# Performance work log

Hardware: AMD Instinct MI355X
Metric: run time of the kernel (lower is better)

Reference implementation:

```python
import jax, jax.numpy as jnp
import numpy as np

B, S, D, K = 32, 1024, 256, 1024
DECAY = 0.99
EPS = 1e-05          # EMA laplace epsilon
LN_EPS = 1e-05       # LayerNorm epsilon
COMMITMENT_COST = 0.25


def setup_inputs() -> dict:
    key = jax.random.key(0)
    k1, k2, k3 = jax.random.split(key, 3)
    inputs = jax.random.normal(k1, (B, S, D), jnp.float32)
    # nn.Embedding init: uniform(-1/K, 1/K)
    weight = jax.random.uniform(k2, (K, D), jnp.float32, -1.0 / K, 1.0 / K)
    ema_w = jax.random.normal(k3, (K, D), jnp.float32)
    ema_cluster_size = jnp.zeros((K,), jnp.float32)
    ln_gamma = jnp.ones((D,), jnp.float32)
    ln_beta = jnp.zeros((D,), jnp.float32)
    return {"inputs": inputs, "weight": weight, "ema_w": ema_w,
            "ema_cluster_size": ema_cluster_size,
            "ln_gamma": ln_gamma, "ln_beta": ln_beta}


def _layernorm(x, g, b):
    mu = jnp.mean(x, axis=-1, keepdims=True)
    var = jnp.mean((x - mu) ** 2, axis=-1, keepdims=True)
    return (x - mu) * jax.lax.rsqrt(var + LN_EPS) * g + b


def reference(inputs, weight, ema_w, ema_cluster_size, ln_gamma, ln_beta):
    flat_input = inputs.reshape(-1, D)          # [N, D] (unnormalized, used for EMA dw)
    feats = _layernorm(flat_input, ln_gamma, ln_beta)  # norm_input in sample()

    # euclidean distances ||f||^2 + ||w||^2 - 2 f w^T  -> [N, K]
    d = (jnp.sum(feats ** 2, axis=1, keepdims=True)
         + jnp.sum(weight ** 2, axis=1)
         - 2.0 * feats @ weight.T)

    sampled_dist = jnp.min(d, axis=1)           # [N]
    idx_flat = jnp.argmin(d, axis=1)            # [N] int

    # faithful reproduction of the source's reordering:
    # argsort per batch row (values in [0,S)) then flat-index into the [N]-long index vector
    order = jnp.argsort(sampled_dist.reshape(B, S), axis=1).reshape(-1)  # [N], values in [0,S)
    enc_idx = idx_flat[order]                   # [N]

    quantized = weight[enc_idx].reshape(B, S, D)

    # ---- EMA codebook update (training path), no gradients ----
    fi = jax.lax.stop_gradient(flat_input)
    counts = jax.ops.segment_sum(jnp.ones((B * S,), jnp.float32), enc_idx,
                                 num_segments=K)                    # encodings.sum(0)
    new_cs = ema_cluster_size * DECAY + (1.0 - DECAY) * counts
    n = jnp.sum(new_cs)
    new_cs = (new_cs + EPS) / (n + K * EPS) * n
    dw = jax.ops.segment_sum(fi, enc_idx, num_segments=K)            # encodings.T @ flat_input
    new_ema_w = jax.lax.stop_gradient(ema_w) * DECAY + (1.0 - DECAY) * dw
    new_weight = new_ema_w / new_cs[:, None]

    # ---- losses (avg=False, loss_type=0) ----
    e_latent = jnp.mean((jax.lax.stop_gradient(quantized) - inputs) ** 2)
    q_latent = jnp.mean((quantized - jax.lax.stop_gradient(inputs)) ** 2)
    loss = q_latent + COMMITMENT_COST * e_latent

    # straight-through estimator
    quantized_st = inputs + jax.lax.stop_gradient(quantized - inputs)

    avg_probs = counts / (B * S)
    perplexity = jnp.exp(-jnp.sum(avg_probs * jnp.log(avg_probs + 1e-10)))

    return quantized_st, loss, perplexity, enc_idx, new_weight, new_ema_w, new_cs
```

## Files before the change

kernel.cpp:

```cpp
#include <hip/hip_runtime.h>
#include <cmath>

#define B_ 32
#define S_ 1024
#define D_ 256
#define K_ 1024
#define N_ (B_*S_)

#define O_Q     0
#define O_LOSS  8388608
#define O_PERP  8388609
#define O_IDX   8388610
#define O_NW    8421378
#define O_NEW   8683522
#define O_NCS   8945666

#define OFF_FH    0ull
#define OFF_WH    16777216ull
#define OFF_BW    17301504ull
#define OFF_BWF   17309696ull
#define OFF_SAMP  17313792ull
#define OFF_IDXF  17575936ull
#define OFF_ENC   17707008ull
#define OFF_CNT   17838080ull
#define OFF_SLOWC 17842176ull
#define OFF_SLOWL 17842240ull
#define OFF_LOSSP 17973312ull
#define OFF_COFF  18235456ull
#define OFF_CUR   18239552ull
#define OFF_ROWL  18243648ull
#define OFF_MUIV  18374720ull
#define OFF_AR    18636864ull
#define OFF_NTOT  18899008ull

#define MARGIN 4e-5f

typedef _Float16 f16x8 __attribute__((ext_vector_type(8)));
typedef _Float16 f16x4 __attribute__((ext_vector_type(4)));
typedef float    f32x4 __attribute__((ext_vector_type(4)));

#define GL16(gp, lp) __builtin_amdgcn_global_load_lds( \
    (const __attribute__((address_space(1))) unsigned int*)(const void*)(gp), \
    (__attribute__((address_space(3))) unsigned int*)(void*)(lp), 16, 0, 0)

__global__ void k_pre(const float* __restrict__ x, const float* __restrict__ gam,
                      const float* __restrict__ bet, _Float16* __restrict__ fh,
                      const float* __restrict__ w, double* __restrict__ Bw,
                      float* __restrict__ Bwf, _Float16* __restrict__ wh,
                      float2* __restrict__ muiv, double* __restrict__ Ar,
                      unsigned* __restrict__ cnt, unsigned* __restrict__ slowC) {
    int lane = threadIdx.x & 63, wv = threadIdx.x >> 6;
    if (blockIdx.x < N_ / 4) {
        int n = blockIdx.x * 4 + wv;
        const float4 xv = ((const float4*)(x + (size_t)n * D_))[lane];
        const float4 gv = ((const float4*)gam)[lane];
        const float4 bv = ((const float4*)bet)[lane];
        float s = xv.x + xv.y + xv.z + xv.w;
        for (int m = 32; m > 0; m >>= 1) s += __shfl_xor(s, m, 64);
        float mu = s * (1.0f / 256.0f);
        float c0 = xv.x - mu, c1 = xv.y - mu, c2 = xv.z - mu, c3 = xv.w - mu;
        float vs = c0 * c0 + c1 * c1 + c2 * c2 + c3 * c3;
        for (int m = 32; m > 0; m >>= 1) vs += __shfl_xor(vs, m, 64);
        float inv = 1.0f / sqrtf(vs * (1.0f / 256.0f) + 1e-5f);
        float f0 = c0 * inv * gv.x + bv.x;
        float f1 = c1 * inv * gv.y + bv.y;
        float f2 = c2 * inv * gv.z + bv.z;
        float f3 = c3 * inv * gv.w + bv.w;
        double a = (double)f0 * f0 + (double)f1 * f1
                 + (double)f2 * f2 + (double)f3 * f3;
        for (int m = 32; m > 0; m >>= 1) a += __shfl_xor(a, m, 64);
        f16x4 o;
        o[0] = (_Float16)f0; o[1] = (_Float16)f1;
        o[2] = (_Float16)f2; o[3] = (_Float16)f3;
        *(f16x4*)&fh[(size_t)n * D_ + lane * 4] = o;
        if (lane == 0) { muiv[n] = make_float2(mu, inv); Ar[n] = a; }
    } else if (blockIdx.x < N_ / 4 + K_ / 4) {
        int k = (blockIdx.x - N_ / 4) * 4 + wv;
        const float4 v = ((const float4*)(w + (size_t)k * D_))[lane];
        double s = (double)v.x * v.x + (double)v.y * v.y
                 + (double)v.z * v.z + (double)v.w * v.w;
        for (int m = 32; m > 0; m >>= 1) s += __shfl_xor(s, m, 64);
        f16x4 o;
        o[0] = (_Float16)v.x; o[1] = (_Float16)v.y;
        o[2] = (_Float16)v.z; o[3] = (_Float16)v.w;
        *(f16x4*)&wh[(size_t)k * D_ + lane * 4] = o;
        if (lane == 0) { Bw[k] = s; Bwf[k] = (float)s; }
    } else {
        int t = threadIdx.x;
#pragma unroll
        for (int i = 0; i < 4; i++) cnt[t + i * 256] = 0u;
        if (t == 0) *slowC = 0u;
    }
}

__launch_bounds__(512, 4)
__global__ void k_phase1(const _Float16* __restrict__ fh, const _Float16* __restrict__ wh,
                         const float* __restrict__ Bwf, float* __restrict__ pq) {
    __shared__ __align__(16) _Float16 sA[3][128][32];
    __shared__ __align__(16) _Float16 sB[3][256][32];

    const int tid = threadIdx.x;
    const int lane = tid & 63;
    const int w = tid >> 6;
    const int wr = w >> 2;
    const int wc = w & 3;
    const int l15 = lane & 15;
    const int g = lane >> 4;
    const int id = blockIdx.x;
    const int grp = (id & 7) * 32 + (id >> 5);
    const int chunk = (id >> 3) & 3;
    const int row0 = grp * 128;
    const int c0 = chunk * 256;

    const int srow = lane >> 2;
    const int scol = (lane & 3) * 8;
    const _Float16* gp[3];
    int lrow[3]; int isA[3];
#pragma unroll
    for (int j = 0; j < 3; j++) {
        int li = w * 3 + j;
        if (li < 8) {
            isA[j] = 1; lrow[j] = li * 16;
            gp[j] = fh + (size_t)(row0 + li * 16 + srow) * 256 + scol;
        } else {
            isA[j] = 0; lrow[j] = (li - 8) * 16;
            gp[j] = wh + (size_t)(c0 + (li - 8) * 16 + srow) * 256 + scol;
        }
    }

    f32x4 acc[4][4];
#pragma unroll
    for (int a = 0; a < 4; a++)
#pragma unroll
        for (int b = 0; b < 4; b++) acc[a][b] = (f32x4){0.f, 0.f, 0.f, 0.f};

#define STAGE(bi, kk) do { \
    const int eoff_ = (kk) * 32; \
    _Pragma("unroll") \
    for (int j_ = 0; j_ < 3; j_++) { \
        if (isA[j_]) GL16(gp[j_] + eoff_, &sA[bi][lrow[j_]][0]); \
        else         GL16(gp[j_] + eoff_, &sB[bi][lrow[j_]][0]); \
    } \
} while (0)

    STAGE(0, 0);
    STAGE(1, 1);
    asm volatile("s_waitcnt vmcnt(3)" ::: "memory");
    __builtin_amdgcn_s_barrier();
    __builtin_amdgcn_sched_barrier(0);

#pragma unroll
    for (int ks = 0; ks < 8; ks++) {
        const int cur = ks % 3;
        if (ks < 6) STAGE((ks + 2) % 3, ks + 2);

        f16x8 cfr[4];
#pragma unroll
        for (int cb = 0; cb < 4; cb++)
            cfr[cb] = *(const f16x8*)&sB[cur][wc * 64 + cb * 16 + l15][g * 8];
        __builtin_amdgcn_s_setprio(1);
#pragma unroll
        for (int rb = 0; rb < 4; rb++) {
            f16x8 rf = *(const f16x8*)&sA[cur][wr * 64 + rb * 16 + l15][g * 8];
#pragma unroll
            for (int cb = 0; cb < 4; cb++)
                acc[cb][rb] = __builtin_amdgcn_mfma_f32_16x16x32_f16(
                    cfr[cb], rf, acc[cb][rb], 0, 0, 0);
        }
        __builtin_amdgcn_s_setprio(0);
        __builtin_amdgcn_sched_barrier(0);

        if (ks < 6)       asm volatile("s_waitcnt vmcnt(3)" ::: "memory");
        else if (ks == 6) asm volatile("s_waitcnt vmcnt(0)" ::: "memory");
        if (ks < 7) {
            __builtin_amdgcn_s_barrier();
            __builtin_amdgcn_sched_barrier(0);
        }
    }
#undef STAGE
    __syncthreads();

    float bwv[4][4];
#pragma unroll
    for (int cb = 0; cb < 4; cb++)
#pragma unroll
        for (int r = 0; r < 4; r++)
            bwv[cb][r] = Bwf[c0 + wc * 64 + cb * 16 + g * 4 + r];

    float* red = (float*)&sA[0][0][0];
#pragma unroll
    for (int rb = 0; rb < 4; rb++) {
        float m1 = 3e38f, m2 = 3e38f; int c1 = 0x7fffffff;
#pragma unroll
        for (int cb = 0; cb < 4; cb++) {
#pragma unroll
            for (int r = 0; r < 4; r++) {
                float sv = fmaf(-2.0f, acc[cb][rb][r], bwv[cb][r]);
                int c = c0 + wc * 64 + cb * 16 + g * 4 + r;
                if (sv < m1 || (sv == m1 && c < c1)) { m2 = m1; m1 = sv; c1 = c; }
                else if (sv < m2) m2 = sv;
            }
        }
#pragma unroll
        for (int msk = 16; msk <= 32; msk <<= 1) {
            float om1 = __shfl_xor(m1, msk, 64);
            float om2 = __shfl_xor(m2, msk, 64);
            int   oc  = __shfl_xor(c1, msk, 64);
            if (om1 < m1 || (om1 == m1 && oc < c1)) {
                m2 = (m1 < om2) ? m1 : om2; m1 = om1; c1 = oc;
            } else {
                m2 = (om1 < m2) ? om1 : m2;
            }
        }
        if (lane < 16) {
            int rl = wr * 64 + rb * 16 + l15;
            int base = (rl * 4 + wc) * 3;
            red[base] = m1; red[base + 1] = m2; ((int*)red)[base + 2] = c1;
        }
    }
    __syncthreads();
    if (tid < 128) {
        float M1 = 3e38f, M2 = 3e38f; int C1 = 0x7fffffff;
        for (int q = 0; q < 4; q++) {
            int base = (tid * 4 + q) * 3;
            float m1 = red[base], m2 = red[base + 1]; int c = ((int*)red)[base + 2];
            if (m1 < M1 || (m1 == M1 && c < C1)) {
                M2 = (M1 < m2) ? M1 : m2; M1 = m1; C1 = c;
            } else {
                M2 = (m1 < M2) ? m1 : M2;
            }
        }
        pq[chunk * N_ + row0 + tid] = M1;
        pq[4 * N_ + chunk * N_ + row0 + tid] = M2;
        ((int*)pq)[8 * N_ + chunk * N_ + row0 + tid] = C1;
    }
}

__global__ void k_phase2(const float* __restrict__ x, const float* __restrict__ gam,
                         const float* __restrict__ bet, const float* __restrict__ w,
                         const double* __restrict__ Bw, const float* __restrict__ pq,
                         const float2* __restrict__ muiv, const double* __restrict__ Ar,
                         double* __restrict__ sampled, int* __restrict__ idxf,
                         unsigned* __restrict__ slowC, int* __restrict__ slowL) {
    int lane = threadIdx.x & 63, wv = threadIdx.x >> 6;
    int n = blockIdx.x * 4 + wv;
    const float* pm1 = pq;
    const float* pm2 = pq + 4 * N_;
    const int*   pc1 = (const int*)pq + 8 * N_;
    float M1 = 3e38f, M2 = 3e38f; int C1 = 0x7fffffff;
#pragma unroll
    for (int c = 0; c < 4; c++) {
        float m1 = pm1[c * N_ + n], m2 = pm2[c * N_ + n]; int cc = pc1[c * N_ + n];
        if (m1 < M1 || (m1 == M1 && cc < C1)) {
            M2 = (M1 < m2) ? M1 : m2; M1 = m1; C1 = cc;
        } else {
            M2 = (m1 < M2) ? m1 : M2;
        }
    }
    if (M2 - M1 <= MARGIN) {
        if (lane == 0) { unsigned p = atomicAdd(slowC, 1u); slowL[p] = n; }
        return;
    }
    float2 mi = muiv[n];
    double mu = mi.x, inv = mi.y;
    double A = Ar[n];
    const float* row = x + (size_t)n * D_;
    const float* wr_ = w + (size_t)C1 * D_;
    double ss = 0.0;
#pragma unroll
    for (int i = 0; i < 4; i++) {
        int d = lane + 64 * i;
        double f = ((double)row[d] - mu) * inv * (double)gam[d] + (double)bet[d];
        ss += f * (double)wr_[d];
    }
    for (int m = 32; m > 0; m >>= 1) ss += __shfl_xor(ss, m, 64);
    if (lane == 0) { sampled[n] = (A + Bw[C1]) - 2.0 * ss; idxf[n] = C1; }
}

__launch_bounds__(256)
__global__ void k_slow(const float* __restrict__ x, const float* __restrict__ gam,
                       const float* __restrict__ bet, const float* __restrict__ w,
                       const double* __restrict__ Bw,
                       const float2* __restrict__ muiv, const double* __restrict__ Ar,
                       const int* __restrict__ slowL, const unsigned* __restrict__ slowC,
                       double* __restrict__ sampled, int* __restrict__ idxf) {
    __shared__ double sf[256];
    __shared__ double bmW[4];
    __shared__ int    bcW[4];
    int tid = threadIdx.x, lane = tid & 63, wv = tid >> 6;
    int cnt = (int)*slowC;
    for (int it = blockIdx.x; it < cnt; it += gridDim.x) {
        int n = slowL[it];
        float2 mi = muiv[n];
        double mu = mi.x, inv = mi.y;
        double A = Ar[n];
        double f = ((double)x[(size_t)n * D_ + tid] - mu) * inv
                   * (double)gam[tid] + (double)bet[tid];
        sf[tid] = f;
        __syncthreads();

        double bm = 1.0e300; int bc = 0x7fffffff;
        for (int r = 0; r < 4; r++) {
            int cc = r * 256 + wv * 64 + lane;
            const float* wr = w + (size_t)cc * D_;
            double acc = 0.0;
#pragma unroll 8
            for (int d4 = 0; d4 < 64; d4++) {
                float4 w4 = *(const float4*)(wr + d4 * 4);
                acc += sf[d4 * 4] * (double)w4.x + sf[d4 * 4 + 1] * (double)w4.y
                     + sf[d4 * 4 + 2] * (double)w4.z + sf[d4 * 4 + 3] * (double)w4.w;
            }
            double dist = (A + Bw[cc]) - 2.0 * acc;
            if (dist < bm) { bm = dist; bc = cc; }
        }
        for (int m = 32; m > 0; m >>= 1) {
            double om = __shfl_xor(bm, m, 64);
            int    oc = __shfl_xor(bc, m, 64);
            if (om < bm || (om == bm && oc < bc)) { bm = om; bc = oc; }
        }
        if (lane == 0) { bmW[wv] = bm; bcW[wv] = bc; }
        __syncthreads();
        if (tid == 0) {
            double M = bmW[0]; int C = bcW[0];
            for (int i = 1; i < 4; i++)
                if (bmW[i] < M || (bmW[i] == M && bcW[i] < C)) { M = bmW[i]; C = bcW[i]; }
            sampled[n] = M; idxf[n] = C;
        }
        __syncthreads();
    }
}

__launch_bounds__(256)
__global__ void k_rank(const double* __restrict__ sampled, const int* __restrict__ idxf,
                       int* __restrict__ enc) {
    __shared__ double val[1024];
    int b = blockIdx.x >> 2;
    int q = blockIdx.x & 3;
    int t = threadIdx.x;
    size_t base = (size_t)b * S_;
#pragma unroll
    for (int e = 0; e < 4; e++)
        val[t + e * 256] = sampled[base + t + e * 256];
    __syncthreads();
    int i = q * 256 + t;
    double vi = val[i];
    int rank = 0;
#pragma unroll 8
    for (int j = 0; j < 1024; j++) {
        double vj = val[j];
        rank += (vj < vi) || (vj == vi && j < i);
    }
    enc[base + rank] = idxf[i];
}

__global__ void k_gather(const float* __restrict__ x, const float* __restrict__ w,
                         const int* __restrict__ enc, float* __restrict__ out,
                         unsigned* __restrict__ cnt, double* __restrict__ lossP) {
    int lane = threadIdx.x & 63, wv = threadIdx.x >> 6;
    int n = blockIdx.x * 4 + wv;
    int e = enc[n];
    const float4 q4 = ((const float4*)(w + (size_t)e * D_))[lane];
    const float4 x4 = ((const float4*)(x + (size_t)n * D_))[lane];
    ((float4*)(out + O_Q + (size_t)n * D_))[lane] = q4;
    double d0 = (double)q4.x - (double)x4.x;
    double d1 = (double)q4.y - (double)x4.y;
    double d2 = (double)q4.z - (double)x4.z;
    double d3 = (double)q4.w - (double)x4.w;
    double ls = d0 * d0 + d1 * d1 + d2 * d2 + d3 * d3;
    for (int m = 32; m > 0; m >>= 1) ls += __shfl_xor(ls, m, 64);
    if (lane == 0) {
        lossP[n] = ls;
        out[O_IDX + n] = (float)e;
        atomicAdd(&cnt[e], 1u);
    }
}

__launch_bounds__(1024)
__global__ void k_scan(const unsigned* __restrict__ cnt, const float* __restrict__ ema_cs,
                       int* __restrict__ coff, int* __restrict__ cur,
                       double* __restrict__ ntotP) {
    __shared__ int tmp[1024];
    __shared__ double redn[16];
    int t = threadIdx.x;
    int my = (int)cnt[t];
    tmp[t] = my;
    double part = (double)(0.99f * ema_cs[t] + 0.01f * (float)my);
    __syncthreads();
    for (int off = 1; off < 1024; off <<= 1) {
        int v = (t >= off) ? tmp[t - off] : 0;
        __syncthreads();
        tmp[t] += v;
        __syncthreads();
    }
    int excl = tmp[t] - my;
    coff[t] = excl;
    cur[t] = excl;
    for (int m = 32; m > 0; m >>= 1) part += __shfl_xor(part, m, 64);
    if ((t & 63) == 0) redn[t >> 6] = part;
    __syncthreads();
    if (t == 0) {
        double s = 0.0;
        for (int i = 0; i < 16; i++) s += redn[i];
        *ntotP = s;
    }
}

__global__ void k_scatter(const int* __restrict__ enc, int* __restrict__ cur,
                          int* __restrict__ rowl) {
    int n = blockIdx.x * 256 + threadIdx.x;
    int e = enc[n];
    int p = atomicAdd(&cur[e], 1);
    rowl[p] = n;
}

__launch_bounds__(256)
__global__ void k_post(const unsigned* __restrict__ cnt, const float* __restrict__ ema_cs,
                       const double* __restrict__ lossP,
                       const int* __restrict__ coff, const int* __restrict__ rowl,
                       const float* __restrict__ x, const float* __restrict__ ema_w,
                       const double* __restrict__ ntotP, float* __restrict__ out) {
    __shared__ double redd[24];
    int tid = threadIdx.x;
    double ntot = *ntotP;

    if (blockIdx.x < K_) {
        int k = blockIdx.x;
        float cs0 = 0.99f * ema_cs[k] + 0.01f * (float)cnt[k];
        double csf = ((double)cs0 + 1e-5) / (ntot + 1024.0 * 1e-5) * ntot;
        int base = coff[k];
        int c = (int)cnt[k];
        float acc = 0.0f;
        int j = 0;
        for (; j + 8 <= c; j += 8) {
            int r[8];
#pragma unroll
            for (int u = 0; u < 8; u++) r[u] = rowl[base + j + u];
            float v[8];
#pragma unroll
            for (int u = 0; u < 8; u++) v[u] = x[(size_t)r[u] * D_ + tid];
#pragma unroll
            for (int u = 0; u < 8; u++) acc += v[u];
        }
        for (; j < c; j++) acc += x[(size_t)rowl[base + j] * D_ + tid];
        size_t idx = (size_t)k * D_ + tid;
        float ne = 0.99f * ema_w[idx] + 0.01f * acc;
        out[O_NEW + idx] = ne;
        out[O_NW + idx] = ne / (float)csf;
    } else {
        for (int i = tid; i < K_; i += 256) {
            float cs0 = 0.99f * ema_cs[i] + 0.01f * (float)cnt[i];
            double c2 = ((double)cs0 + 1e-5) / (ntot + 1024.0 * 1e-5) * ntot;
            out[O_NCS + i] = (float)c2;
        }
        double ent = 0.0;
        for (int i = tid; i < K_; i += 256) {
            double p = (double)cnt[i] / 32768.0;
            ent += -p * log(p + 1e-10);
        }
        for (int m = 32; m > 0; m >>= 1) ent += __shfl_xor(ent, m, 64);
        if ((tid & 63) == 0) redd[8 + (tid >> 6)] = ent;
        double ls = 0.0;
        for (int i = tid; i < N_; i += 256) ls += lossP[i];
        for (int m = 32; m > 0; m >>= 1) ls += __shfl_xor(ls, m, 64);
        if ((tid & 63) == 0) redd[16 + (tid >> 6)] = ls;
        __syncthreads();
        if (tid == 0) {
            double e = redd[8] + redd[9] + redd[10] + redd[11];
            double l = redd[16] + redd[17] + redd[18] + redd[19];
            out[O_PERP] = (float)exp(e);
            out[O_LOSS] = (float)(1.25 * l / 8388608.0);
        }
    }
}

extern "C" void kernel_launch(void* const* d_in, const int* in_sizes, int n_in,
                              void* d_out, int out_size, void* d_ws, size_t ws_size,
                              hipStream_t stream) {
    (void)in_sizes; (void)n_in; (void)out_size; (void)ws_size;
    const float* x      = (const float*)d_in[0];
    const float* w      = (const float*)d_in[1];
    const float* ema_w  = (const float*)d_in[2];
    const float* ema_cs = (const float*)d_in[3];
    const float* g      = (const float*)d_in[4];
    const float* bt     = (const float*)d_in[5];
    float* out = (float*)d_out;
    char* ws = (char*)d_ws;

    _Float16* fh = (_Float16*)(ws + OFF_FH);
    _Float16* wh = (_Float16*)(ws + OFF_WH);
    double* Bw   = (double*)(ws + OFF_BW);
    float*  Bwf  = (float*)(ws + OFF_BWF);
    double* samp = (double*)(ws + OFF_SAMP);
    int*    idxf = (int*)(ws + OFF_IDXF);
    int*    enc  = (int*)(ws + OFF_ENC);
    unsigned* cnt = (unsigned*)(ws + OFF_CNT);
    unsigned* slowC = (unsigned*)(ws + OFF_SLOWC);
    int*    slowL = (int*)(ws + OFF_SLOWL);
    double* lossP = (double*)(ws + OFF_LOSSP);
    int*    coff  = (int*)(ws + OFF_COFF);
    int*    cur   = (int*)(ws + OFF_CUR);
    int*    rowl  = (int*)(ws + OFF_ROWL);
    float2* muiv  = (float2*)(ws + OFF_MUIV);
    double* Ar    = (double*)(ws + OFF_AR);
    double* ntotP = (double*)(ws + OFF_NTOT);

    k_pre<<<N_ / 4 + K_ / 4 + 1, 256, 0, stream>>>(x, g, bt, fh, w, Bw, Bwf, wh,
                                                   muiv, Ar, cnt, slowC);
    k_phase1<<<1024, 512, 0, stream>>>(fh, wh, Bwf, out);
    k_phase2<<<N_ / 4, 256, 0, stream>>>(x, g, bt, w, Bw, out, muiv, Ar,
                                         samp, idxf, slowC, slowL);
    k_slow<<<2048, 256, 0, stream>>>(x, g, bt, w, Bw, muiv, Ar, slowL, slowC, samp, idxf);
    k_rank<<<B_ * 4, 256, 0, stream>>>(samp, idxf, enc);
    k_gather<<<N_ / 4, 256, 0, stream>>>(x, w, enc, out, cnt, lossP);
    k_scan<<<1, 1024, 0, stream>>>(cnt, ema_cs, coff, cur, ntotP);
    k_scatter<<<N_ / 256, 256, 0, stream>>>(enc, cur, rowl);
    k_post<<<K_ + 1, 256, 0, stream>>>(cnt, ema_cs, lossP, coff, rowl, x, ema_w,
                                       ntotP, out);
}
```

Measured before the change: 279.5 us.

## Fold slow-path rescoring into phase2 and merge scatter into scan kernel

The separate k_slow kernel, its atomic worklist and counter are removed. Ambiguous rows (top-2 gap within the margin) are now rescored exactly in fp64 by the same wavefront in k_phase2, with each lane scanning 16 codewords. The k_scatter kernel is folded into the single-block scan kernel, which now uses LDS atomics for the bucket cursors. This cuts two kernel launches and the global atomics, but a wave that hits the slow path stalls its block, and the scatter of 32K rows now runs serially in one workgroup.

```diff
diff --git a/kernel.cpp b/kernel.cpp
--- a/kernel.cpp
+++ b/kernel.cpp
@@ -23,11 +23,8 @@
 #define OFF_IDXF  17575936ull
 #define OFF_ENC   17707008ull
 #define OFF_CNT   17838080ull
-#define OFF_SLOWC 17842176ull
-#define OFF_SLOWL 17842240ull
 #define OFF_LOSSP 17973312ull
 #define OFF_COFF  18235456ull
-#define OFF_CUR   18239552ull
 #define OFF_ROWL  18243648ull
 #define OFF_MUIV  18374720ull
 #define OFF_AR    18636864ull
@@ -48,7 +45,7 @@
                       const float* __restrict__ w, double* __restrict__ Bw,
                       float* __restrict__ Bwf, _Float16* __restrict__ wh,
                       float2* __restrict__ muiv, double* __restrict__ Ar,
-                      unsigned* __restrict__ cnt, unsigned* __restrict__ slowC) {
+                      unsigned* __restrict__ cnt) {
     int lane = threadIdx.x & 63, wv = threadIdx.x >> 6;
     if (blockIdx.x < N_ / 4) {
         int n = blockIdx.x * 4 + wv;
@@ -89,7 +86,6 @@
         int t = threadIdx.x;
 #pragma unroll
         for (int i = 0; i < 4; i++) cnt[t + i * 256] = 0u;
-        if (t == 0) *slowC = 0u;
     }
 }
 
@@ -236,12 +232,13 @@
     }
 }
 
+__launch_bounds__(256)
 __global__ void k_phase2(const float* __restrict__ x, const float* __restrict__ gam,
                          const float* __restrict__ bet, const float* __restrict__ w,
                          const double* __restrict__ Bw, const float* __restrict__ pq,
                          const float2* __restrict__ muiv, const double* __restrict__ Ar,
-                         double* __restrict__ sampled, int* __restrict__ idxf,
-                         unsigned* __restrict__ slowC, int* __restrict__ slowL) {
+                         double* __restrict__ sampled, int* __restrict__ idxf) {
+    __shared__ double sf[4][256];
     int lane = threadIdx.x & 63, wv = threadIdx.x >> 6;
     int n = blockIdx.x * 4 + wv;
     const float* pm1 = pq;
@@ -257,60 +254,40 @@
             M2 = (m1 < M2) ? m1 : M2;
         }
     }
-    if (M2 - M1 <= MARGIN) {
-        if (lane == 0) { unsigned p = atomicAdd(slowC, 1u); slowL[p] = n; }
-        return;
-    }
     float2 mi = muiv[n];
     double mu = mi.x, inv = mi.y;
     double A = Ar[n];
     const float* row = x + (size_t)n * D_;
-    const float* wr_ = w + (size_t)C1 * D_;
-    double ss = 0.0;
-#pragma unroll
-    for (int i = 0; i < 4; i++) {
-        int d = lane + 64 * i;
-        double f = ((double)row[d] - mu) * inv * (double)gam[d] + (double)bet[d];
-        ss += f * (double)wr_[d];
-    }
-    for (int m = 32; m > 0; m >>= 1) ss += __shfl_xor(ss, m, 64);
-    if (lane == 0) { sampled[n] = (A + Bw[C1]) - 2.0 * ss; idxf[n] = C1; }
-}
-
-__launch_bounds__(256)
-__global__ void k_slow(const float* __restrict__ x, const float* __restrict__ gam,
-                       const float* __restrict__ bet, const float* __restrict__ w,
-                       const double* __restrict__ Bw,
-                       const float2* __restrict__ muiv, const double* __restrict__ Ar,
-                       const int* __restrict__ slowL, const unsigned* __restrict__ slowC,
-                       double* __restrict__ sampled, int* __restrict__ idxf) {
-    __shared__ double sf[256];
-    __shared__ double bmW[4];
-    __shared__ int    bcW[4];
-    int tid = threadIdx.x, lane = tid & 63, wv = tid >> 6;
-    int cnt = (int)*slowC;
-    for (int it = blockIdx.x; it < cnt; it += gridDim.x) {
-        int n = slowL[it];
-        float2 mi = muiv[n];
-        double mu = mi.x, inv = mi.y;
-        double A = Ar[n];
-        double f = ((double)x[(size_t)n * D_ + tid] - mu) * inv
-                   * (double)gam[tid] + (double)bet[tid];
-        sf[tid] = f;
-        __syncthreads();
-
+
+    if (M2 - M1 > MARGIN) {
+        const float* wr_ = w + (size_t)C1 * D_;
+        double ss = 0.0;
+#pragma unroll
+        for (int i = 0; i < 4; i++) {
+            int d = lane + 64 * i;
+            double f = ((double)row[d] - mu) * inv * (double)gam[d] + (double)bet[d];
+            ss += f * (double)wr_[d];
+        }
+        for (int m = 32; m > 0; m >>= 1) ss += __shfl_xor(ss, m, 64);
+        if (lane == 0) { sampled[n] = (A + Bw[C1]) - 2.0 * ss; idxf[n] = C1; }
+    } else {
+#pragma unroll
+        for (int i = 0; i < 4; i++) {
+            int d = lane + 64 * i;
+            sf[wv][d] = ((double)row[d] - mu) * inv * (double)gam[d] + (double)bet[d];
+        }
         double bm = 1.0e300; int bc = 0x7fffffff;
-        for (int r = 0; r < 4; r++) {
-            int cc = r * 256 + wv * 64 + lane;
+        for (int k = 0; k < 16; k++) {
+            int cc = lane * 16 + k;
             const float* wr = w + (size_t)cc * D_;
-            double acc = 0.0;
+            double acc2 = 0.0;
 #pragma unroll 8
             for (int d4 = 0; d4 < 64; d4++) {
                 float4 w4 = *(const float4*)(wr + d4 * 4);
-                acc += sf[d4 * 4] * (double)w4.x + sf[d4 * 4 + 1] * (double)w4.y
-                     + sf[d4 * 4 + 2] * (double)w4.z + sf[d4 * 4 + 3] * (double)w4.w;
+                acc2 += sf[wv][d4 * 4] * (double)w4.x + sf[wv][d4 * 4 + 1] * (double)w4.y
+                      + sf[wv][d4 * 4 + 2] * (double)w4.z + sf[wv][d4 * 4 + 3] * (double)w4.w;
             }
-            double dist = (A + Bw[cc]) - 2.0 * acc;
+            double dist = (A + Bw[cc]) - 2.0 * acc2;
             if (dist < bm) { bm = dist; bc = cc; }
         }
         for (int m = 32; m > 0; m >>= 1) {
@@ -318,15 +295,7 @@
             int    oc = __shfl_xor(bc, m, 64);
             if (om < bm || (om == bm && oc < bc)) { bm = om; bc = oc; }
         }
-        if (lane == 0) { bmW[wv] = bm; bcW[wv] = bc; }
-        __syncthreads();
-        if (tid == 0) {
-            double M = bmW[0]; int C = bcW[0];
-            for (int i = 1; i < 4; i++)
-                if (bmW[i] < M || (bmW[i] == M && bcW[i] < C)) { M = bmW[i]; C = bcW[i]; }
-            sampled[n] = M; idxf[n] = C;
-        }
-        __syncthreads();
+        if (lane == 0) { sampled[n] = bm; idxf[n] = bc; }
     }
 }
 
@@ -376,10 +345,11 @@
 }
 
 __launch_bounds__(1024)
-__global__ void k_scan(const unsigned* __restrict__ cnt, const float* __restrict__ ema_cs,
-                       int* __restrict__ coff, int* __restrict__ cur,
-                       double* __restrict__ ntotP) {
+__global__ void k_scansc(const unsigned* __restrict__ cnt, const float* __restrict__ ema_cs,
+                         const int* __restrict__ enc, int* __restrict__ coff,
+                         int* __restrict__ rowl, double* __restrict__ ntotP) {
     __shared__ int tmp[1024];
+    __shared__ int curL[1024];
     __shared__ double redn[16];
     int t = threadIdx.x;
     int my = (int)cnt[t];
@@ -394,7 +364,7 @@
     }
     int excl = tmp[t] - my;
     coff[t] = excl;
-    cur[t] = excl;
+    curL[t] = excl;
     for (int m = 32; m > 0; m >>= 1) part += __shfl_xor(part, m, 64);
     if ((t & 63) == 0) redn[t >> 6] = part;
     __syncthreads();
@@ -403,14 +373,12 @@
         for (int i = 0; i < 16; i++) s += redn[i];
         *ntotP = s;
     }
-}
-
-__global__ void k_scatter(const int* __restrict__ enc, int* __restrict__ cur,
-                          int* __restrict__ rowl) {
-    int n = blockIdx.x * 256 + threadIdx.x;
-    int e = enc[n];
-    int p = atomicAdd(&cur[e], 1);
-    rowl[p] = n;
+    for (int it = 0; it < 32; it++) {
+        int i = it * 1024 + t;
+        int e = enc[i];
+        int p = atomicAdd(&curL[e], 1);
+        rowl[p] = i;
+    }
 }
 
 __launch_bounds__(256)
@@ -494,26 +462,20 @@
     int*    idxf = (int*)(ws + OFF_IDXF);
     int*    enc  = (int*)(ws + OFF_ENC);
     unsigned* cnt = (unsigned*)(ws + OFF_CNT);
-    unsigned* slowC = (unsigned*)(ws + OFF_SLOWC);
-    int*    slowL = (int*)(ws + OFF_SLOWL);
     double* lossP = (double*)(ws + OFF_LOSSP);
     int*    coff  = (int*)(ws + OFF_COFF);
-    int*    cur   = (int*)(ws + OFF_CUR);
     int*    rowl  = (int*)(ws + OFF_ROWL);
     float2* muiv  = (float2*)(ws + OFF_MUIV);
     double* Ar    = (double*)(ws + OFF_AR);
     double* ntotP = (double*)(ws + OFF_NTOT);
 
     k_pre<<<N_ / 4 + K_ / 4 + 1, 256, 0, stream>>>(x, g, bt, fh, w, Bw, Bwf, wh,
-                                                   muiv, Ar, cnt, slowC);
+                                                   muiv, Ar, cnt);
     k_phase1<<<1024, 512, 0, stream>>>(fh, wh, Bwf, out);
-    k_phase2<<<N_ / 4, 256, 0, stream>>>(x, g, bt, w, Bw, out, muiv, Ar,
-                                         samp, idxf, slowC, slowL);
-    k_slow<<<2048, 256, 0, stream>>>(x, g, bt, w, Bw, muiv, Ar, slowL, slowC, samp, idxf);
+    k_phase2<<<N_ / 4, 256, 0, stream>>>(x, g, bt, w, Bw, out, muiv, Ar, samp, idxf);
     k_rank<<<B_ * 4, 256, 0, stream>>>(samp, idxf, enc);
     k_gather<<<N_ / 4, 256, 0, stream>>>(x, w, enc, out, cnt, lossP);
-    k_scan<<<1, 1024, 0, stream>>>(cnt, ema_cs, coff, cur, ntotP);
-    k_scatter<<<N_ / 256, 256, 0, stream>>>(enc, cur, rowl);
+    k_scansc<<<1, 1024, 0, stream>>>(cnt, ema_cs, enc, coff, rowl, ntotP);
     k_post<<<K_ + 1, 256, 0, stream>>>(cnt, ema_cs, lossP, coff, rowl, x, ema_w,
                                        ntotP, out);
 }
```

Measured after the change: 377.0 us. 34.9% more time.
